# Kernel optimization log

Hardware: AMD Instinct MI355X
Metric: run time of the kernel (lower is better)

## Reference

```python
import jax, jax.numpy as jnp
import numpy as np

jax.config.update("jax_enable_x64", True)  # Q16.16 int64 fixed-point arithmetic requires 64-bit ints

F = 16                 # FixedPointConfig.COMPUTE_FRAC_BITS (Q16.16)
ONE = 1 << F

B, S, D_IN, D_OUT = 2, 2048, 4096, 4096


def setup_inputs() -> dict:
    key = jax.random.key(0)
    k1, k2 = jax.random.split(key)
    x = jax.random.normal(k1, (B, S, D_IN), dtype=jnp.float32)
    weight = jax.random.normal(k2, (D_OUT, D_IN), dtype=jnp.float32)
    return {"x": x, "weight": weight}


def _to_fixed(x):
    # to_fixed_point: float -> Q16.16 int64
    return jnp.round(x * ONE).astype(jnp.int64)


def _activation_quant_fixed(xf):
    # per-token 8-bit quant/dequant, all in Q16.16 integer arithmetic
    max_vals = jnp.max(jnp.abs(xf), axis=-1, keepdims=True)
    min_val = int(1e-5 * ONE)  # == 0 at frac_bits=16 (faithful to source)
    max_vals = jnp.maximum(max_vals, min_val)
    target_max = 127 << F
    # fixed_div(target_max, max_vals, F, F, F): (a << F) // b
    scale = (target_max << F) // max_vals
    # fixed_mul(x, scale, F, F, F): (a*b) >> F  (arithmetic shift == floor-div)
    x_scaled = (xf * scale) >> F
    x_clamped = jnp.clip(x_scaled, -(128 << F), 127 << F)
    # fixed_reciprocal(scale, F, F): (1 << 2F) // scale
    scale_inv = (1 << (2 * F)) // scale
    return (x_clamped * scale_inv) >> F


def reference(x, weight):
    # --- quantize_weights() ---
    wf = _to_fixed(weight)                                   # Q16.16
    mean_abs = jnp.sum(jnp.abs(wf)) // wf.size               # fixed_mean (Q16.16 scalar)
    # fixed_div(wf, mean_abs, F, F, 0) -> integer-valued; round+clamp to {-1,0,1}
    w_ternary = jnp.clip(wf // mean_abs, -1, 1).astype(jnp.int8)

    # --- forward ---
    xq = _activation_quant_fixed(_to_fixed(x))               # [B,S,D] Q16.16 int64
    xq2 = xq.reshape(-1, D_IN)
    # Ternary GEMM replacing the per-output-feature masked-sum loop.
    # |xq| <= 128<<16 ~ 8.4e6 and K=4096 => |acc| <= 3.4e10 < 2^53, so a
    acc = jnp.dot(xq2.astype(jnp.float64), w_ternary.astype(jnp.float64).T)
    out = jnp.round(acc).astype(jnp.int64)
    out = out.astype(jnp.int32).astype(jnp.int64)            # replicate torch .to(int32) wrap
    scale_inv = (1 << (2 * F)) // mean_abs                   # fixed_reciprocal of weight_scale
    out = (out * scale_inv) >> F                             # fixed_mul dequant/rescale
    out = out.reshape(B, S, D_OUT)
    return out.astype(jnp.float32) / ONE                     # from_fixed_point
```

## Files before the change

kernel.cpp:

```cpp
#include <hip/hip_runtime.h>
#include <stdint.h>

typedef int v4i  __attribute__((ext_vector_type(4)));
typedef int v16i __attribute__((ext_vector_type(16)));

static constexpr int Mdim = 4096;
static constexpr int Ndim = 4096;
static constexpr int Kdim = 4096;

static constexpr size_t TILE_BYTES  = 128u * 4096u;
static constexpr size_t OFF_ROWPAR  = 4096;
static constexpr size_t OFF_BT      = 1u << 20;
static constexpr size_t OFF_A0      = 17u << 20;
static constexpr size_t PLANE_BYTES = 16u << 20;

__device__ __forceinline__ void gload16(const void* g, void* l) {
  __builtin_amdgcn_global_load_lds(
      (const __attribute__((address_space(1))) char*)g,
      (__attribute__((address_space(3))) char*)l, 16, 0, 0);
}

__global__ void k_wsum(const float* __restrict__ w, unsigned long long* __restrict__ ws) {
  int tid = blockIdx.x * blockDim.x + threadIdx.x;
  int stride = gridDim.x * blockDim.x;
  const float4* w4 = (const float4*)w;
  const int n4 = (Ndim * Kdim) / 4;
  unsigned long long s = 0;
  for (int i = tid; i < n4; i += stride) {
    float4 v = w4[i];
    long long a = llrintf(v.x * 65536.f);
    long long b = llrintf(v.y * 65536.f);
    long long c = llrintf(v.z * 65536.f);
    long long d = llrintf(v.w * 65536.f);
    s += (unsigned long long)(a < 0 ? -a : a) + (unsigned long long)(b < 0 ? -b : b)
       + (unsigned long long)(c < 0 ? -c : c) + (unsigned long long)(d < 0 ? -d : d);
  }
  #pragma unroll
  for (int off = 32; off > 0; off >>= 1) s += __shfl_down(s, off, 64);
  if ((threadIdx.x & 63) == 0) atomicAdd(ws, s);
}

__global__ void k_scalars(unsigned long long* ws) {
  unsigned long long s = ws[0];
  long long mean_abs = (long long)(s >> 24);
  if (mean_abs < 1) mean_abs = 1;
  long long siw = (long long)((1ULL << 32) / (unsigned long long)mean_abs);
  ((long long*)ws)[1] = siw;
  ((long long*)ws)[2] = mean_abs;
}

__global__ void k_tern(const float* __restrict__ w, const long long* __restrict__ scal,
                       int8_t* __restrict__ bt) {
  int t = blockIdx.x * 256 + threadIdx.x;
  long long mean_abs = scal[2];
  int nt = t >> 15;
  int kc = (t >> 7) & 255;
  int r  = t & 127;
  int row = nt * 128 + r;
  const float4* src = (const float4*)(w + (size_t)row * Kdim + kc * 16);
  int words[4];
  #pragma unroll
  for (int j = 0; j < 4; ++j) {
    float4 v = src[j];
    float e0 = v.x, e1 = v.y, e2 = v.z, e3 = v.w;
    int wrd = 0;
    long long f;
    f = llrintf(e0 * 65536.f); wrd |= ((f < 0 ? -1 : (f >= mean_abs ? 1 : 0)) & 0xff);
    f = llrintf(e1 * 65536.f); wrd |= ((f < 0 ? -1 : (f >= mean_abs ? 1 : 0)) & 0xff) << 8;
    f = llrintf(e2 * 65536.f); wrd |= ((f < 0 ? -1 : (f >= mean_abs ? 1 : 0)) & 0xff) << 16;
    f = llrintf(e3 * 65536.f); wrd |= ((f < 0 ? -1 : (f >= mean_abs ? 1 : 0)) & 0xff) << 24;
    words[j] = wrd;
  }
  *(int4*)(bt + (size_t)nt * TILE_BYTES + (size_t)kc * 2048 + (size_t)r * 16) =
      make_int4(words[0], words[1], words[2], words[3]);
}

__global__ void k_rowmax(const float* __restrict__ x, long long* __restrict__ rowpar) {
  int m = blockIdx.x;
  const float4* xr = (const float4*)(x + (size_t)m * Kdim);
  long long mx = 0;
  #pragma unroll
  for (int j = 0; j < 4; ++j) {
    float4 v = xr[j * 256 + threadIdx.x];
    long long a = llrintf(v.x * 65536.f); a = a < 0 ? -a : a; mx = a > mx ? a : mx;
    long long b = llrintf(v.y * 65536.f); b = b < 0 ? -b : b; mx = b > mx ? b : mx;
    long long c = llrintf(v.z * 65536.f); c = c < 0 ? -c : c; mx = c > mx ? c : mx;
    long long d = llrintf(v.w * 65536.f); d = d < 0 ? -d : d; mx = d > mx ? d : mx;
  }
  #pragma unroll
  for (int off = 32; off > 0; off >>= 1) {
    long long o = __shfl_down(mx, off, 64);
    mx = o > mx ? o : mx;
  }
  __shared__ long long red[4];
  if ((threadIdx.x & 63) == 0) red[threadIdx.x >> 6] = mx;
  __syncthreads();
  if (threadIdx.x == 0) {
    long long m0 = red[0];
    m0 = red[1] > m0 ? red[1] : m0;
    m0 = red[2] > m0 ? red[2] : m0;
    m0 = red[3] > m0 ? red[3] : m0;
    if (m0 < 1) m0 = 1;
    long long scale = (long long)((127ULL << 32) / (unsigned long long)m0);
    long long sinv  = (long long)((1ULL << 32) / (unsigned long long)scale);
    rowpar[2 * m]     = scale;
    rowpar[2 * m + 1] = sinv;
  }
}

__global__ void k_actq(const float* __restrict__ x, const long long* __restrict__ rowpar,
                       int8_t* __restrict__ a0, int8_t* __restrict__ a1, int8_t* __restrict__ a2) {
  int t = blockIdx.x * 256 + threadIdx.x;
  int mt = t >> 15;
  int kc = (t >> 7) & 255;
  int r  = t & 127;
  int m = mt * 128 + r;
  long long scale = rowpar[2 * m];
  long long sinv  = rowpar[2 * m + 1];
  const float4* src = (const float4*)(x + (size_t)m * Kdim + kc * 16);
  int w0[4], w1[4], w2[4];
  #pragma unroll
  for (int j = 0; j < 4; ++j) {
    float4 v = src[j];
    float e[4] = {v.x, v.y, v.z, v.w};
    int r0 = 0, r1 = 0, r2 = 0;
    #pragma unroll
    for (int q = 0; q < 4; ++q) {
      long long xf = llrintf(e[q] * 65536.f);
      long long xs = (xf * scale) >> 16;
      if (xs < -8388608LL) xs = -8388608LL;
      else if (xs > 8323072LL) xs = 8323072LL;
      int xq = (int)((xs * sinv) >> 16);
      int l0 = ((xq + 128) & 255) - 128;
      int tt = (xq - l0) >> 8;
      int l1 = ((tt + 128) & 255) - 128;
      int l2 = (tt - l1) >> 8;
      r0 |= (l0 & 0xff) << (8 * q);
      r1 |= (l1 & 0xff) << (8 * q);
      r2 |= (l2 & 0xff) << (8 * q);
    }
    w0[j] = r0; w1[j] = r1; w2[j] = r2;
  }
  size_t idx = (size_t)mt * TILE_BYTES + (size_t)kc * 2048 + (size_t)r * 16;
  *(int4*)(a0 + idx) = make_int4(w0[0], w0[1], w0[2], w0[3]);
  *(int4*)(a1 + idx) = make_int4(w1[0], w1[1], w1[2], w1[3]);
  *(int4*)(a2 + idx) = make_int4(w2[0], w2[1], w2[2], w2[3]);
}

__launch_bounds__(512, 2)
__global__ void k_gemm(const int8_t* __restrict__ a0, const int8_t* __restrict__ a1,
                       const int8_t* __restrict__ a2, const int8_t* __restrict__ bt,
                       const long long* __restrict__ scal, float* __restrict__ out) {
  __shared__ __attribute__((aligned(16))) char lds[2][4][8192];
  int bx = blockIdx.x;
  int mt = bx >> 5;
  int nt = bx & 31;
  int tid  = threadIdx.x;
  int lane = tid & 63;
  int w    = tid >> 6;
  int wm   = w >> 1;
  int wn   = w & 1;

  const char* planes[4];
  planes[0] = (const char*)a0 + (size_t)mt * TILE_BYTES;
  planes[1] = (const char*)a1 + (size_t)mt * TILE_BYTES;
  planes[2] = (const char*)a2 + (size_t)mt * TILE_BYTES;
  planes[3] = (const char*)bt + (size_t)nt * TILE_BYTES;

  v16i acc[2][3] = {};

  auto STAGE = [&](int buf, int kt) {
    #pragma unroll
    for (int p = 0; p < 4; ++p)
      gload16(planes[p] + (size_t)kt * 8192 + (size_t)tid * 16, &lds[buf][p][tid * 16]);
  };

  auto COMPUTE = [&](int buf) {
    #pragma unroll
    for (int ks = 0; ks < 2; ++ks) {
      const int koff = (ks * 2 + (lane >> 5)) * 2048;
      v4i bfrag[2], afrag[3];
      #pragma unroll
      for (int nj = 0; nj < 2; ++nj)
        bfrag[nj] = *(const v4i*)&lds[buf][3][koff + (wn * 64 + nj * 32 + (lane & 31)) * 16];
      #pragma unroll
      for (int p = 0; p < 3; ++p)
        afrag[p] = *(const v4i*)&lds[buf][p][koff + (wm * 32 + (lane & 31)) * 16];
      #pragma unroll
      for (int nj = 0; nj < 2; ++nj)
        #pragma unroll
        for (int p = 0; p < 3; ++p)
          acc[nj][p] = __builtin_amdgcn_mfma_i32_32x32x32_i8(afrag[p], bfrag[nj], acc[nj][p], 0, 0, 0);
    }
  };

  STAGE(0, 0);
  __syncthreads();
  const int NT = Kdim / 64;
  for (int kt = 0; kt < NT; ++kt) {
    int cur = kt & 1;
    if (kt + 1 < NT) STAGE(cur ^ 1, kt + 1);
    COMPUTE(cur);
    __syncthreads();
  }

  long long siw = scal[1];
  int m0 = mt * 128 + wm * 32;
  int n0 = nt * 128 + wn * 64;
  #pragma unroll
  for (int nj = 0; nj < 2; ++nj) {
    #pragma unroll
    for (int rg = 0; rg < 16; ++rg) {
      unsigned u = (unsigned)acc[nj][0][rg]
                 + ((unsigned)acc[nj][1][rg] << 8)
                 + ((unsigned)acc[nj][2][rg] << 16);
      long long v = ((long long)(int)u * siw) >> 16;
      int row = (rg & 3) + 8 * (rg >> 2) + 4 * (lane >> 5);
      int col = nj * 32 + (lane & 31);
      out[(size_t)(m0 + row) * Ndim + (n0 + col)] = (float)v * (1.f / 65536.f);
    }
  }
}

extern "C" void kernel_launch(void* const* d_in, const int* in_sizes, int n_in,
                              void* d_out, int out_size, void* d_ws, size_t ws_size,
                              hipStream_t stream) {
  const float* x = (const float*)d_in[0];
  const float* w = (const float*)d_in[1];
  float* out = (float*)d_out;
  char* ws = (char*)d_ws;

  unsigned long long* scal = (unsigned long long*)ws;
  long long* rowpar = (long long*)(ws + OFF_ROWPAR);
  int8_t* bt = (int8_t*)(ws + OFF_BT);
  int8_t* a0 = (int8_t*)(ws + OFF_A0);
  int8_t* a1 = a0 + PLANE_BYTES;
  int8_t* a2 = a1 + PLANE_BYTES;

  hipMemsetAsync(ws, 0, 64, stream);
  k_wsum<<<1024, 256, 0, stream>>>(w, scal);
  k_scalars<<<1, 1, 0, stream>>>(scal);
  k_tern<<<4096, 256, 0, stream>>>(w, (const long long*)scal, bt);
  k_rowmax<<<4096, 256, 0, stream>>>(x, rowpar);
  k_actq<<<4096, 256, 0, stream>>>(x, rowpar, a0, a1, a2);
  k_gemm<<<1024, 512, 0, stream>>>(a0, a1, a2, bt, (const long long*)scal, out);
}
```

Before: 427.9 us.

## Deepen GEMM LDS pipeline to four stages with explicit vmcnt waits and setprio

The GEMM main loop moves from double buffering with a full __syncthreads per step to a four-buffer ring that prefetches three k-tiles ahead. It uses manual s_waitcnt vmcnt counts and bare s_barrier, and raises wave priority around the MFMA block. Launch bounds drop the two-blocks-per-CU hint because LDS doubles to 128KB. The preprocessing kernels also switch from 64-bit llrintf arithmetic to 32-bit rintf/int math to cut int64 ALU cost. The risks are lower occupancy (one block per CU) and correctness depending on the hand-tuned vmcnt values.

```diff
diff --git a/kernel.cpp b/kernel.cpp
--- a/kernel.cpp
+++ b/kernel.cpp
@@ -28,12 +28,13 @@
   unsigned long long s = 0;
   for (int i = tid; i < n4; i += stride) {
     float4 v = w4[i];
-    long long a = llrintf(v.x * 65536.f);
-    long long b = llrintf(v.y * 65536.f);
-    long long c = llrintf(v.z * 65536.f);
-    long long d = llrintf(v.w * 65536.f);
-    s += (unsigned long long)(a < 0 ? -a : a) + (unsigned long long)(b < 0 ? -b : b)
-       + (unsigned long long)(c < 0 ? -c : c) + (unsigned long long)(d < 0 ? -d : d);
+    int a = (int)rintf(v.x * 65536.f);
+    int b = (int)rintf(v.y * 65536.f);
+    int c = (int)rintf(v.z * 65536.f);
+    int d = (int)rintf(v.w * 65536.f);
+    unsigned u = (unsigned)(a < 0 ? -a : a) + (unsigned)(b < 0 ? -b : b)
+               + (unsigned)(c < 0 ? -c : c) + (unsigned)(d < 0 ? -d : d);
+    s += u;
   }
   #pragma unroll
   for (int off = 32; off > 0; off >>= 1) s += __shfl_down(s, off, 64);
@@ -52,7 +53,7 @@
 __global__ void k_tern(const float* __restrict__ w, const long long* __restrict__ scal,
                        int8_t* __restrict__ bt) {
   int t = blockIdx.x * 256 + threadIdx.x;
-  long long mean_abs = scal[2];
+  int mean_abs = (int)scal[2];
   int nt = t >> 15;
   int kc = (t >> 7) & 255;
   int r  = t & 127;
@@ -62,13 +63,14 @@
   #pragma unroll
   for (int j = 0; j < 4; ++j) {
     float4 v = src[j];
-    float e0 = v.x, e1 = v.y, e2 = v.z, e3 = v.w;
+    float e[4] = {v.x, v.y, v.z, v.w};
     int wrd = 0;
-    long long f;
-    f = llrintf(e0 * 65536.f); wrd |= ((f < 0 ? -1 : (f >= mean_abs ? 1 : 0)) & 0xff);
-    f = llrintf(e1 * 65536.f); wrd |= ((f < 0 ? -1 : (f >= mean_abs ? 1 : 0)) & 0xff) << 8;
-    f = llrintf(e2 * 65536.f); wrd |= ((f < 0 ? -1 : (f >= mean_abs ? 1 : 0)) & 0xff) << 16;
-    f = llrintf(e3 * 65536.f); wrd |= ((f < 0 ? -1 : (f >= mean_abs ? 1 : 0)) & 0xff) << 24;
+    #pragma unroll
+    for (int q = 0; q < 4; ++q) {
+      int f = (int)rintf(e[q] * 65536.f);
+      int tv = (f >= mean_abs ? 1 : 0) - (f < 0 ? 1 : 0);
+      wrd |= (tv & 0xff) << (8 * q);
+    }
     words[j] = wrd;
   }
   *(int4*)(bt + (size_t)nt * TILE_BYTES + (size_t)kc * 2048 + (size_t)r * 16) =
@@ -78,25 +80,25 @@
 __global__ void k_rowmax(const float* __restrict__ x, long long* __restrict__ rowpar) {
   int m = blockIdx.x;
   const float4* xr = (const float4*)(x + (size_t)m * Kdim);
-  long long mx = 0;
+  int mx = 0;
   #pragma unroll
   for (int j = 0; j < 4; ++j) {
     float4 v = xr[j * 256 + threadIdx.x];
-    long long a = llrintf(v.x * 65536.f); a = a < 0 ? -a : a; mx = a > mx ? a : mx;
-    long long b = llrintf(v.y * 65536.f); b = b < 0 ? -b : b; mx = b > mx ? b : mx;
-    long long c = llrintf(v.z * 65536.f); c = c < 0 ? -c : c; mx = c > mx ? c : mx;
-    long long d = llrintf(v.w * 65536.f); d = d < 0 ? -d : d; mx = d > mx ? d : mx;
+    int a = (int)rintf(v.x * 65536.f); a = a < 0 ? -a : a; mx = a > mx ? a : mx;
+    int b = (int)rintf(v.y * 65536.f); b = b < 0 ? -b : b; mx = b > mx ? b : mx;
+    int c = (int)rintf(v.z * 65536.f); c = c < 0 ? -c : c; mx = c > mx ? c : mx;
+    int d = (int)rintf(v.w * 65536.f); d = d < 0 ? -d : d; mx = d > mx ? d : mx;
   }
   #pragma unroll
   for (int off = 32; off > 0; off >>= 1) {
-    long long o = __shfl_down(mx, off, 64);
+    int o = __shfl_down(mx, off, 64);
     mx = o > mx ? o : mx;
   }
-  __shared__ long long red[4];
+  __shared__ int red[4];
   if ((threadIdx.x & 63) == 0) red[threadIdx.x >> 6] = mx;
   __syncthreads();
   if (threadIdx.x == 0) {
-    long long m0 = red[0];
+    int m0 = red[0];
     m0 = red[1] > m0 ? red[1] : m0;
     m0 = red[2] > m0 ? red[2] : m0;
     m0 = red[3] > m0 ? red[3] : m0;
@@ -126,14 +128,14 @@
     int r0 = 0, r1 = 0, r2 = 0;
     #pragma unroll
     for (int q = 0; q < 4; ++q) {
-      long long xf = llrintf(e[q] * 65536.f);
-      long long xs = (xf * scale) >> 16;
-      if (xs < -8388608LL) xs = -8388608LL;
-      else if (xs > 8323072LL) xs = 8323072LL;
-      int xq = (int)((xs * sinv) >> 16);
-      int l0 = ((xq + 128) & 255) - 128;
+      int xf = (int)rintf(e[q] * 65536.f);
+      int xs = (int)(((long long)xf * scale) >> 16);
+      xs = xs < -8388608 ? -8388608 : xs;
+      xs = xs > 8323072 ? 8323072 : xs;
+      int xq = (int)(((long long)xs * sinv) >> 16);
+      int l0 = (int)(signed char)(xq & 0xff);
       int tt = (xq - l0) >> 8;
-      int l1 = ((tt + 128) & 255) - 128;
+      int l1 = (int)(signed char)(tt & 0xff);
       int l2 = (tt - l1) >> 8;
       r0 |= (l0 & 0xff) << (8 * q);
       r1 |= (l1 & 0xff) << (8 * q);
@@ -147,11 +149,11 @@
   *(int4*)(a2 + idx) = make_int4(w2[0], w2[1], w2[2], w2[3]);
 }
 
-__launch_bounds__(512, 2)
+__launch_bounds__(512)
 __global__ void k_gemm(const int8_t* __restrict__ a0, const int8_t* __restrict__ a1,
                        const int8_t* __restrict__ a2, const int8_t* __restrict__ bt,
                        const long long* __restrict__ scal, float* __restrict__ out) {
-  __shared__ __attribute__((aligned(16))) char lds[2][4][8192];
+  __shared__ __attribute__((aligned(16))) char lds[4][4][8192];
   int bx = blockIdx.x;
   int mt = bx >> 5;
   int nt = bx & 31;
@@ -186,22 +188,37 @@
       #pragma unroll
       for (int p = 0; p < 3; ++p)
         afrag[p] = *(const v4i*)&lds[buf][p][koff + (wm * 32 + (lane & 31)) * 16];
+      __builtin_amdgcn_s_setprio(1);
       #pragma unroll
       for (int nj = 0; nj < 2; ++nj)
         #pragma unroll
         for (int p = 0; p < 3; ++p)
           acc[nj][p] = __builtin_amdgcn_mfma_i32_32x32x32_i8(afrag[p], bfrag[nj], acc[nj][p], 0, 0, 0);
+      __builtin_amdgcn_s_setprio(0);
     }
   };
 
-  STAGE(0, 0);
-  __syncthreads();
   const int NT = Kdim / 64;
-  for (int kt = 0; kt < NT; ++kt) {
-    int cur = kt & 1;
-    if (kt + 1 < NT) STAGE(cur ^ 1, kt + 1);
-    COMPUTE(cur);
-    __syncthreads();
+  STAGE(0, 0); STAGE(1, 1); STAGE(2, 2);
+  asm volatile("s_waitcnt vmcnt(8)" ::: "memory");
+  __builtin_amdgcn_s_barrier();
+  asm volatile("" ::: "memory");
+
+  for (int t = 0; t < NT; ++t) {
+    COMPUTE(t & 3);
+    asm volatile("" ::: "memory");
+    if (t + 3 < NT) {
+      STAGE((t + 3) & 3, t + 3);
+      asm volatile("s_waitcnt vmcnt(8)" ::: "memory");
+    } else if (t == NT - 3) {
+      asm volatile("s_waitcnt vmcnt(4)" ::: "memory");
+    } else if (t == NT - 2) {
+      asm volatile("s_waitcnt vmcnt(0)" ::: "memory");
+    }
+    if (t < NT - 1) {
+      __builtin_amdgcn_s_barrier();
+      asm volatile("" ::: "memory");
+    }
   }
 
   long long siw = scal[1];
```

New measurement: 429.9 us. No clear change (+0.5%).
